# Kernel tuning notes

Measured on AMD Instinct MI355X. Metric: run time of the kernel, lower is better.

Reference implementation:

```python
import jax, jax.numpy as jnp
import numpy as np

N_NODES = 50000
N_EDGES = 600000
FEAT = 128
HID = 128
OUT = 64
N_LAYERS = 4
N_GRAPHS = 128
BN_EPS = 1e-5


def setup_inputs() -> dict:
    key = jax.random.key(0)
    ks = jax.random.split(key, 16)
    x = jax.random.normal(ks[0], (N_NODES, FEAT), dtype=jnp.float32)
    edge_index = jax.random.randint(ks[1], (2, N_EDGES), 0, N_NODES, dtype=jnp.int32)
    batch = jnp.sort(jax.random.randint(ks[2], (N_NODES,), 0, N_GRAPHS, dtype=jnp.int32))
    s = 1.0 / np.sqrt(HID)
    # feat_dim == hidden_dim so all per-layer MLP weights stack to [L, HID, HID]
    W1 = jax.random.normal(ks[3], (N_LAYERS, HID, HID), dtype=jnp.float32) * s
    b1 = jnp.zeros((N_LAYERS, HID), dtype=jnp.float32)
    W2 = jax.random.normal(ks[4], (N_LAYERS, HID, HID), dtype=jnp.float32) * s
    b2 = jnp.zeros((N_LAYERS, HID), dtype=jnp.float32)
    gamma = jnp.ones((N_LAYERS, HID), dtype=jnp.float32)
    beta = jnp.zeros((N_LAYERS, HID), dtype=jnp.float32)
    Wf1 = jax.random.normal(ks[5], (HID, HID), dtype=jnp.float32) * s
    bf1 = jnp.zeros((HID,), dtype=jnp.float32)
    Wf2 = jax.random.normal(ks[6], (HID, OUT), dtype=jnp.float32) * s
    bf2 = jnp.zeros((OUT,), dtype=jnp.float32)
    return {"x": x, "edge_index": edge_index, "batch": batch,
            "W1": W1, "b1": b1, "W2": W2, "b2": b2,
            "gamma": gamma, "beta": beta,
            "Wf1": Wf1, "bf1": bf1, "Wf2": Wf2, "bf2": bf2}


def reference(x, edge_index, batch, W1, b1, W2, b2, gamma, beta, Wf1, bf1, Wf2, bf2):
    src, dst = edge_index[0], edge_index[1]
    h = x
    for l in range(N_LAYERS):
        # GINConv (eps=0): h_i <- MLP(h_i + sum_{j in N(i)} h_j)
        agg = jax.ops.segment_sum(h[src], dst, num_segments=N_NODES)
        h = h + agg
        h = jnp.matmul(jax.nn.relu(jnp.matmul(h, W1[l]) + b1[l]), W2[l]) + b2[l]
        # BatchNorm1d (training mode: batch stats over node dim)
        mean = jnp.mean(h, axis=0)
        var = jnp.var(h, axis=0)
        h = (h - mean) * jax.lax.rsqrt(var + BN_EPS) * gamma[l] + beta[l]
        h = jax.nn.relu(h)
    # global_add_pool over graph ids
    g = jax.ops.segment_sum(h, batch, num_segments=N_GRAPHS)  # [G, HID]
    out = jnp.matmul(jax.nn.relu(jnp.matmul(g, Wf1) + bf1), Wf2) + bf2  # [G, OUT]
    return out
```

## Files before the change

### kernel.cpp

```cpp
#include <hip/hip_runtime.h>

#define NN 50000
#define NE 600000
#define HD 128
#define OUTF 64
#define NL 4
#define NG 128
#define BN_EPS 1e-5f
#define NSB 196

typedef __attribute__((ext_vector_type(8))) short short8v;
typedef __attribute__((ext_vector_type(4))) float float4v;

#define LDSW 136

__device__ inline unsigned short f2bf(float f) {
    unsigned int u = __float_as_uint(f);
    return (unsigned short)((u + 0x7FFF + ((u >> 16) & 1)) >> 16);
}
__device__ inline float bf2f(short s) {
    return __uint_as_float(((unsigned int)(unsigned short)s) << 16);
}

__global__ __launch_bounds__(256) void pack_w_kernel(
    const float* __restrict__ W1, const float* __restrict__ W2,
    short* __restrict__ wpack, float* __restrict__ stats4)
{
    int gid = blockIdx.x * 256 + threadIdx.x;
    if (gid < 256)
        reinterpret_cast<float4*>(stats4)[gid] = (float4){0.f, 0.f, 0.f, 0.f};
    int l  = gid & 63;
    int kb = (gid >> 6) & 3;
    int nt = (gid >> 8) & 7;
    int w  = gid >> 11;
    const float* W = (w & 1) ? (W2 + (size_t)(w >> 1) * HD * HD)
                             : (W1 + (size_t)(w >> 1) * HD * HD);
    int col  = nt * 16 + (l & 15);
    int krow = kb * 32 + (l >> 4) * 8;
    short* o = wpack + (size_t)w * 16384 + ((size_t)(nt * 4 + kb) * 64 + l) * 8;
    #pragma unroll
    for (int i = 0; i < 8; i++)
        o[i] = (short)f2bf(W[(size_t)(krow + i) * HD + col]);
}

__global__ __launch_bounds__(256) void cvt_bf16_kernel(
    const float* __restrict__ x, short* __restrict__ hb)
{
    int idx = blockIdx.x * 256 + threadIdx.x;
    if (idx >= NN * 32) return;
    float4 v = reinterpret_cast<const float4*>(x)[idx];
    short4 o = make_short4((short)f2bf(v.x), (short)f2bf(v.y),
                           (short)f2bf(v.z), (short)f2bf(v.w));
    reinterpret_cast<short4*>(hb)[idx] = o;
}

__global__ __launch_bounds__(512) void layer_kernel(
    const short* __restrict__ hb, const int* __restrict__ row_ptr,
    const int* __restrict__ csr, const short* __restrict__ wp1,
    const float* __restrict__ b1, const short* __restrict__ wp2,
    const float* __restrict__ b2, short* __restrict__ Cb,
    float* __restrict__ sums, float* __restrict__ sumsq)
{
    __shared__ __align__(16) short As[64 * LDSW];
    const int t = threadIdx.x;
    const int row0 = blockIdx.x * 64;

    {
        const int ng = t >> 4;
        const int c8 = (t & 15) * 8;
        #pragma unroll
        for (int it = 0; it < 2; it++) {
            int lr = it * 32 + ng;
            int n = row0 + lr;
            float acc[8] = {0, 0, 0, 0, 0, 0, 0, 0};
            if (n < NN) {
                short8v s = *reinterpret_cast<const short8v*>(&hb[(size_t)n * HD + c8]);
                #pragma unroll
                for (int i = 0; i < 8; i++) acc[i] = bf2f(s[i]);
                int p = row_ptr[n], pe = row_ptr[n + 1];
                for (; p + 2 <= pe; p += 2) {
                    int s0 = csr[p], s1 = csr[p + 1];
                    short8v a = *reinterpret_cast<const short8v*>(&hb[(size_t)s0 * HD + c8]);
                    short8v b = *reinterpret_cast<const short8v*>(&hb[(size_t)s1 * HD + c8]);
                    #pragma unroll
                    for (int i = 0; i < 8; i++) acc[i] += bf2f(a[i]) + bf2f(b[i]);
                }
                if (p < pe) {
                    short8v a = *reinterpret_cast<const short8v*>(&hb[(size_t)csr[p] * HD + c8]);
                    #pragma unroll
                    for (int i = 0; i < 8; i++) acc[i] += bf2f(a[i]);
                }
            }
            short8v o;
            #pragma unroll
            for (int i = 0; i < 8; i++) o[i] = (short)f2bf(acc[i]);
            *reinterpret_cast<short8v*>(&As[lr * LDSW + c8]) = o;
        }
    }
    __syncthreads();

    const int wv = t >> 6, l = t & 63;
    const int l16 = l & 15, lhi = l >> 4;
    const int wrow = (wv >> 1) * 16;
    const int nc0 = (wv & 1) * 4;

    short8v a[4];
    #pragma unroll
    for (int kb = 0; kb < 4; kb++)
        a[kb] = *reinterpret_cast<const short8v*>(&As[(wrow + l16) * LDSW + kb * 32 + lhi * 8]);
    __syncthreads();

    float4v acc[4];
    #pragma unroll
    for (int q = 0; q < 4; q++) acc[q] = (float4v){0.f, 0.f, 0.f, 0.f};
    {
        const short8v* wp = reinterpret_cast<const short8v*>(wp1);
        #pragma unroll
        for (int q = 0; q < 4; q++) {
            int nt = nc0 + q;
            #pragma unroll
            for (int kb = 0; kb < 4; kb++) {
                short8v b = wp[(nt * 4 + kb) * 64 + l];
                acc[q] = __builtin_amdgcn_mfma_f32_16x16x32_bf16(a[kb], b, acc[q], 0, 0, 0);
            }
        }
    }
    #pragma unroll
    for (int q = 0; q < 4; q++) {
        int nt = nc0 + q;
        float bnt = b1[nt * 16 + l16];
        #pragma unroll
        for (int j = 0; j < 4; j++) {
            float v = fmaxf(acc[q][j] + bnt, 0.f);
            As[(wrow + lhi * 4 + j) * LDSW + nt * 16 + l16] = (short)f2bf(v);
        }
    }
    __syncthreads();

    #pragma unroll
    for (int kb = 0; kb < 4; kb++)
        a[kb] = *reinterpret_cast<const short8v*>(&As[(wrow + l16) * LDSW + kb * 32 + lhi * 8]);

    #pragma unroll
    for (int q = 0; q < 4; q++) acc[q] = (float4v){0.f, 0.f, 0.f, 0.f};
    {
        const short8v* wp = reinterpret_cast<const short8v*>(wp2);
        #pragma unroll
        for (int q = 0; q < 4; q++) {
            int nt = nc0 + q;
            #pragma unroll
            for (int kb = 0; kb < 4; kb++) {
                short8v b = wp[(nt * 4 + kb) * 64 + l];
                acc[q] = __builtin_amdgcn_mfma_f32_16x16x32_bf16(a[kb], b, acc[q], 0, 0, 0);
            }
        }
    }

    __syncthreads();
    float* redS = reinterpret_cast<float*>(As);
    float* redQ = redS + 4 * HD;
    #pragma unroll
    for (int q = 0; q < 4; q++) {
        int nt = nc0 + q;
        float bnt = b2[nt * 16 + l16];
        float snt = 0.f, qnt = 0.f;
        #pragma unroll
        for (int j = 0; j < 4; j++) {
            int r = row0 + wrow + lhi * 4 + j;
            if (r < NN) {
                float v = acc[q][j] + bnt;
                Cb[(size_t)r * HD + nt * 16 + l16] = (short)f2bf(v);
                snt += v; qnt += v * v;
            }
        }
        snt += __shfl_xor(snt, 16); snt += __shfl_xor(snt, 32);
        qnt += __shfl_xor(qnt, 16); qnt += __shfl_xor(qnt, 32);
        if (lhi == 0) {
            redS[(wv >> 1) * HD + nt * 16 + l16] = snt;
            redQ[(wv >> 1) * HD + nt * 16 + l16] = qnt;
        }
    }
    __syncthreads();
    if (t < HD) {
        float ss = redS[0 * HD + t] + redS[1 * HD + t] + redS[2 * HD + t] + redS[3 * HD + t];
        float qq = redQ[0 * HD + t] + redQ[1 * HD + t] + redQ[2 * HD + t] + redQ[3 * HD + t];
        atomicAdd(&sums[t], ss);
        atomicAdd(&sumsq[t], qq);
    }
}

__global__ __launch_bounds__(256) void deg_hist_kernel(
    const int* __restrict__ dst, int* __restrict__ deg)
{
    int e = blockIdx.x * 256 + threadIdx.x;
    if (e < NE) atomicAdd(&deg[dst[e]], 1);
}

__global__ __launch_bounds__(256) void scan_partial_kernel(
    const int* __restrict__ deg, int* __restrict__ bsum)
{
    __shared__ int sd[256];
    int t = threadIdx.x;
    int i = blockIdx.x * 256 + t;
    sd[t] = (i < NN) ? deg[i] : 0;
    __syncthreads();
    for (int o = 128; o > 0; o >>= 1) {
        if (t < o) sd[t] += sd[t + o];
        __syncthreads();
    }
    if (t == 0) bsum[blockIdx.x] = sd[0];
}

__global__ __launch_bounds__(256) void scan_bsums_kernel(
    const int* __restrict__ bsum, int* __restrict__ boff)
{
    __shared__ int sd[256];
    int t = threadIdx.x;
    int v = (t < NSB) ? bsum[t] : 0;
    sd[t] = v;
    __syncthreads();
    for (int o = 1; o < 256; o <<= 1) {
        int x = (t >= o) ? sd[t - o] : 0;
        __syncthreads();
        sd[t] += x;
        __syncthreads();
    }
    if (t < NSB) boff[t] = sd[t] - v;
}

__global__ __launch_bounds__(256) void scan_final_kernel(
    const int* __restrict__ deg, const int* __restrict__ boff,
    int* __restrict__ row_ptr, int* __restrict__ cursor)
{
    __shared__ int sd[256];
    int t = threadIdx.x;
    int i = blockIdx.x * 256 + t;
    int v = (i < NN) ? deg[i] : 0;
    sd[t] = v;
    __syncthreads();
    for (int o = 1; o < 256; o <<= 1) {
        int x = (t >= o) ? sd[t - o] : 0;
        __syncthreads();
        sd[t] += x;
        __syncthreads();
    }
    int excl = sd[t] - v + boff[blockIdx.x];
    if (i < NN) { row_ptr[i] = excl; cursor[i] = excl; }
    if (i == NN - 1) row_ptr[NN] = excl + v;
}

__global__ __launch_bounds__(256) void fill_csr_kernel(
    const int* __restrict__ src, const int* __restrict__ dst,
    int* __restrict__ cursor, int* __restrict__ csr)
{
    int e = blockIdx.x * 256 + threadIdx.x;
    if (e >= NE) return;
    int p = atomicAdd(&cursor[dst[e]], 1);
    csr[p] = src[e];
}

__global__ __launch_bounds__(256) void bn_apply_kernel(
    const short* __restrict__ Cb, const float* __restrict__ sums,
    const float* __restrict__ sumsq, const float* __restrict__ gamma,
    const float* __restrict__ beta, short* __restrict__ hb)
{
    __shared__ float sscale[HD];
    __shared__ float sshift[HD];
    int t = threadIdx.x;
    if (t < HD) {
        const float invN = 1.f / (float)NN;
        float mean = sums[t] * invN;
        float var = sumsq[t] * invN - mean * mean;
        float inv = rsqrtf(var + BN_EPS);
        float sc = gamma[t] * inv;
        sscale[t] = sc;
        sshift[t] = beta[t] - mean * sc;
    }
    __syncthreads();
    int idx = blockIdx.x * 256 + t;
    if (idx >= NN * 16) return;
    short8v v = reinterpret_cast<const short8v*>(Cb)[idx];
    int c0 = (idx & 15) * 8;
    short8v o;
    #pragma unroll
    for (int i = 0; i < 8; i++) {
        float f = fmaxf(bf2f(v[i]) * sscale[c0 + i] + sshift[c0 + i], 0.f);
        o[i] = (short)f2bf(f);
    }
    reinterpret_cast<short8v*>(hb)[idx] = o;
}

__global__ __launch_bounds__(256) void pool_kernel_v3(
    const short* __restrict__ hb, const int* __restrict__ batch,
    float* __restrict__ g)
{
    const int gr = blockIdx.x;
    int lo = 0, hi = NN;
    while (lo < hi) { int m = (lo + hi) >> 1; if (batch[m] < gr) lo = m + 1; else hi = m; }
    const int start = lo;
    hi = NN;
    while (lo < hi) { int m = (lo + hi) >> 1; if (batch[m] <= gr) lo = m + 1; else hi = m; }
    const int end = lo;

    const int cg = threadIdx.x & 15;
    const int rg = threadIdx.x >> 4;
    float acc[8] = {0, 0, 0, 0, 0, 0, 0, 0};
    for (int r = start + rg; r < end; r += 16) {
        short8v v = *reinterpret_cast<const short8v*>(&hb[(size_t)r * HD + cg * 8]);
        #pragma unroll
        for (int i = 0; i < 8; i++) acc[i] += bf2f(v[i]);
    }
    __shared__ float red[16][HD];
    #pragma unroll
    for (int i = 0; i < 8; i++) red[rg][cg * 8 + i] = acc[i];
    __syncthreads();
    if (threadIdx.x < HD) {
        float s = 0.f;
        #pragma unroll
        for (int k = 0; k < 16; k++) s += red[k][threadIdx.x];
        g[gr * HD + threadIdx.x] = s;
    }
}

__global__ __launch_bounds__(128) void final_kernel(
    const float* __restrict__ g, const float* __restrict__ Wf1,
    const float* __restrict__ bf1, const float* __restrict__ Wf2,
    const float* __restrict__ bf2, float* __restrict__ out)
{
    __shared__ float gr[HD];
    __shared__ float yr[HD];
    int r = blockIdx.x, c = threadIdx.x;
    gr[c] = g[r * HD + c];
    __syncthreads();
    float acc = bf1[c];
    for (int k = 0; k < HD; k++) acc += gr[k] * Wf1[k * HD + c];
    yr[c] = fmaxf(acc, 0.f);
    __syncthreads();
    if (c < OUTF) {
        float o = bf2[c];
        for (int k = 0; k < HD; k++) o += yr[k] * Wf2[k * OUTF + c];
        out[r * OUTF + c] = o;
    }
}

extern "C" void kernel_launch(void* const* d_in, const int* in_sizes, int n_in,
                              void* d_out, int out_size, void* d_ws, size_t ws_size,
                              hipStream_t stream)
{
    const float* x     = (const float*)d_in[0];
    const int*   ei    = (const int*)  d_in[1];
    const int*   batch = (const int*)  d_in[2];
    const float* W1    = (const float*)d_in[3];
    const float* b1    = (const float*)d_in[4];
    const float* W2    = (const float*)d_in[5];
    const float* b2    = (const float*)d_in[6];
    const float* gamma = (const float*)d_in[7];
    const float* beta  = (const float*)d_in[8];
    const float* Wf1   = (const float*)d_in[9];
    const float* bf1   = (const float*)d_in[10];
    const float* Wf2   = (const float*)d_in[11];
    const float* bf2   = (const float*)d_in[12];
    float* out = (float*)d_out;

    float* ws   = (float*)d_ws;
    const size_t BIG = (size_t)NN * HD;
    short* Cb   = (short*)ws;
    short* hb   = (short*)(ws + BIG);
    float* smal = ws + 3 * BIG;
    float* stats4 = smal;
    float* gpool  = smal + 2048;
    int* ip      = (int*)(smal + 65536);
    int* deg     = ip;
    int* row_ptr = ip + NN;
    int* cursor  = row_ptr + NN + 1;
    int* bsum    = cursor + NN;
    int* boff    = bsum + 256;
    int* csr     = boff + 256;
    short* wpack = (short*)(csr + NE);

    const int* src = ei;
    const int* dst = ei + NE;

    const int layer_grid = (NN + 63) / 64;
    const int cvt_grid  = (NN * 32 + 255) / 256;
    const int bn_grid   = (NN * 16 + 255) / 256;
    const int edge_grid = (NE + 255) / 256;

    pack_w_kernel<<<64, 256, 0, stream>>>(W1, W2, wpack, stats4);
    cvt_bf16_kernel<<<cvt_grid, 256, 0, stream>>>(x, hb);
    hipMemsetAsync(deg, 0, NN * sizeof(int), stream);
    deg_hist_kernel<<<edge_grid, 256, 0, stream>>>(dst, deg);
    scan_partial_kernel<<<NSB, 256, 0, stream>>>(deg, bsum);
    scan_bsums_kernel<<<1, 256, 0, stream>>>(bsum, boff);
    scan_final_kernel<<<NSB, 256, 0, stream>>>(deg, boff, row_ptr, cursor);
    fill_csr_kernel<<<edge_grid, 256, 0, stream>>>(src, dst, cursor, csr);

    for (int l = 0; l < NL; l++) {
        float* sums  = stats4 + l * 256;
        float* sumsq = sums + 128;
        layer_kernel<<<layer_grid, 512, 0, stream>>>(
            hb, row_ptr, csr,
            wpack + (size_t)(l * 2 + 0) * 16384, b1 + l * HD,
            wpack + (size_t)(l * 2 + 1) * 16384, b2 + l * HD,
            Cb, sums, sumsq);
        bn_apply_kernel<<<bn_grid, 256, 0, stream>>>(
            Cb, sums, sumsq, gamma + l * HD, beta + l * HD, hb);
    }

    pool_kernel_v3<<<NG, 256, 0, stream>>>(hb, batch, gpool);
    final_kernel<<<NG, 128, 0, stream>>>(gpool, Wf1, bf1, Wf2, bf2, out);
}
```

Before: 339.4 us.

## Fuse BatchNorm apply and ReLU into next layer's gather and pooling

Removes the separate bn_apply kernel. The BN scale/shift plus ReLU is now applied on the fly when the next layer gathers neighbour features, and in the pooling kernel for the last layer. Layer outputs ping-pong between two buffers. This saves a full read/write pass over the node features per layer and four kernel launches. In exchange, the affine+ReLU is recomputed once per edge in the gather, adding ALU work to a memory-bound loop.

```diff
diff --git a/kernel.cpp b/kernel.cpp
--- a/kernel.cpp
+++ b/kernel.cpp
@@ -54,41 +54,70 @@
     reinterpret_cast<short4*>(hb)[idx] = o;
 }
 
+template<bool BN>
 __global__ __launch_bounds__(512) void layer_kernel(
-    const short* __restrict__ hb, const int* __restrict__ row_ptr,
-    const int* __restrict__ csr, const short* __restrict__ wp1,
-    const float* __restrict__ b1, const short* __restrict__ wp2,
-    const float* __restrict__ b2, short* __restrict__ Cb,
-    float* __restrict__ sums, float* __restrict__ sumsq)
+    const short* __restrict__ inb, const float* __restrict__ stats_prev,
+    const float* __restrict__ gamma_p, const float* __restrict__ beta_p,
+    const int* __restrict__ row_ptr, const int* __restrict__ csr,
+    const short* __restrict__ wp1, const float* __restrict__ b1,
+    const short* __restrict__ wp2, const float* __restrict__ b2,
+    short* __restrict__ Cb, float* __restrict__ sums, float* __restrict__ sumsq)
 {
     __shared__ __align__(16) short As[64 * LDSW];
+    __shared__ float sscale[HD];
+    __shared__ float sshift[HD];
     const int t = threadIdx.x;
     const int row0 = blockIdx.x * 64;
 
+    float sc[8], sh[8];
+    const int c8 = (t & 15) * 8;
+    if (BN) {
+        if (t < HD) {
+            const float invN = 1.f / (float)NN;
+            float mean = stats_prev[t] * invN;
+            float var = stats_prev[HD + t] * invN - mean * mean;
+            float inv = rsqrtf(var + BN_EPS);
+            float s = gamma_p[t] * inv;
+            sscale[t] = s;
+            sshift[t] = beta_p[t] - mean * s;
+        }
+        __syncthreads();
+        #pragma unroll
+        for (int i = 0; i < 8; i++) { sc[i] = sscale[c8 + i]; sh[i] = sshift[c8 + i]; }
+    }
+
     {
         const int ng = t >> 4;
-        const int c8 = (t & 15) * 8;
         #pragma unroll
         for (int it = 0; it < 2; it++) {
             int lr = it * 32 + ng;
             int n = row0 + lr;
             float acc[8] = {0, 0, 0, 0, 0, 0, 0, 0};
             if (n < NN) {
-                short8v s = *reinterpret_cast<const short8v*>(&hb[(size_t)n * HD + c8]);
+                short8v s = *reinterpret_cast<const short8v*>(&inb[(size_t)n * HD + c8]);
                 #pragma unroll
-                for (int i = 0; i < 8; i++) acc[i] = bf2f(s[i]);
+                for (int i = 0; i < 8; i++)
+                    acc[i] = BN ? fmaxf(bf2f(s[i]) * sc[i] + sh[i], 0.f) : bf2f(s[i]);
                 int p = row_ptr[n], pe = row_ptr[n + 1];
                 for (; p + 2 <= pe; p += 2) {
                     int s0 = csr[p], s1 = csr[p + 1];
-                    short8v a = *reinterpret_cast<const short8v*>(&hb[(size_t)s0 * HD + c8]);
-                    short8v b = *reinterpret_cast<const short8v*>(&hb[(size_t)s1 * HD + c8]);
-                    #pragma unroll
-                    for (int i = 0; i < 8; i++) acc[i] += bf2f(a[i]) + bf2f(b[i]);
+                    short8v a = *reinterpret_cast<const short8v*>(&inb[(size_t)s0 * HD + c8]);
+                    short8v b = *reinterpret_cast<const short8v*>(&inb[(size_t)s1 * HD + c8]);
+                    if (BN) {
+                        #pragma unroll
+                        for (int i = 0; i < 8; i++)
+                            acc[i] += fmaxf(bf2f(a[i]) * sc[i] + sh[i], 0.f)
+                                    + fmaxf(bf2f(b[i]) * sc[i] + sh[i], 0.f);
+                    } else {
+                        #pragma unroll
+                        for (int i = 0; i < 8; i++) acc[i] += bf2f(a[i]) + bf2f(b[i]);
+                    }
                 }
                 if (p < pe) {
-                    short8v a = *reinterpret_cast<const short8v*>(&hb[(size_t)csr[p] * HD + c8]);
+                    short8v a = *reinterpret_cast<const short8v*>(&inb[(size_t)csr[p] * HD + c8]);
                     #pragma unroll
-                    for (int i = 0; i < 8; i++) acc[i] += bf2f(a[i]);
+                    for (int i = 0; i < 8; i++)
+                        acc[i] += BN ? fmaxf(bf2f(a[i]) * sc[i] + sh[i], 0.f) : bf2f(a[i]);
                 }
             }
             short8v o;
@@ -259,41 +288,25 @@
     csr[p] = src[e];
 }
 
-__global__ __launch_bounds__(256) void bn_apply_kernel(
-    const short* __restrict__ Cb, const float* __restrict__ sums,
-    const float* __restrict__ sumsq, const float* __restrict__ gamma,
-    const float* __restrict__ beta, short* __restrict__ hb)
+__global__ __launch_bounds__(256) void pool_kernel_v4(
+    const short* __restrict__ Cb, const float* __restrict__ stats,
+    const float* __restrict__ gamma_p, const float* __restrict__ beta_p,
+    const int* __restrict__ batch, float* __restrict__ g)
 {
     __shared__ float sscale[HD];
     __shared__ float sshift[HD];
-    int t = threadIdx.x;
+    const int t = threadIdx.x;
     if (t < HD) {
         const float invN = 1.f / (float)NN;
-        float mean = sums[t] * invN;
-        float var = sumsq[t] * invN - mean * mean;
+        float mean = stats[t] * invN;
+        float var = stats[HD + t] * invN - mean * mean;
         float inv = rsqrtf(var + BN_EPS);
-        float sc = gamma[t] * inv;
-        sscale[t] = sc;
-        sshift[t] = beta[t] - mean * sc;
-    }
-    __syncthreads();
-    int idx = blockIdx.x * 256 + t;
-    if (idx >= NN * 16) return;
-    short8v v = reinterpret_cast<const short8v*>(Cb)[idx];
-    int c0 = (idx & 15) * 8;
-    short8v o;
-    #pragma unroll
-    for (int i = 0; i < 8; i++) {
-        float f = fmaxf(bf2f(v[i]) * sscale[c0 + i] + sshift[c0 + i], 0.f);
-        o[i] = (short)f2bf(f);
-    }
-    reinterpret_cast<short8v*>(hb)[idx] = o;
-}
-
-__global__ __launch_bounds__(256) void pool_kernel_v3(
-    const short* __restrict__ hb, const int* __restrict__ batch,
-    float* __restrict__ g)
-{
+        float s = gamma_p[t] * inv;
+        sscale[t] = s;
+        sshift[t] = beta_p[t] - mean * s;
+    }
+    __syncthreads();
+
     const int gr = blockIdx.x;
     int lo = 0, hi = NN;
     while (lo < hi) { int m = (lo + hi) >> 1; if (batch[m] < gr) lo = m + 1; else hi = m; }
@@ -302,23 +315,28 @@
     while (lo < hi) { int m = (lo + hi) >> 1; if (batch[m] <= gr) lo = m + 1; else hi = m; }
     const int end = lo;
 
-    const int cg = threadIdx.x & 15;
-    const int rg = threadIdx.x >> 4;
+    const int cg = t & 15;
+    const int rg = t >> 4;
+    float sc[8], sh[8];
+    #pragma unroll
+    for (int i = 0; i < 8; i++) { sc[i] = sscale[cg * 8 + i]; sh[i] = sshift[cg * 8 + i]; }
+
     float acc[8] = {0, 0, 0, 0, 0, 0, 0, 0};
     for (int r = start + rg; r < end; r += 16) {
-        short8v v = *reinterpret_cast<const short8v*>(&hb[(size_t)r * HD + cg * 8]);
-        #pragma unroll
-        for (int i = 0; i < 8; i++) acc[i] += bf2f(v[i]);
+        short8v v = *reinterpret_cast<const short8v*>(&Cb[(size_t)r * HD + cg * 8]);
+        #pragma unroll
+        for (int i = 0; i < 8; i++)
+            acc[i] += fmaxf(bf2f(v[i]) * sc[i] + sh[i], 0.f);
     }
     __shared__ float red[16][HD];
     #pragma unroll
     for (int i = 0; i < 8; i++) red[rg][cg * 8 + i] = acc[i];
     __syncthreads();
-    if (threadIdx.x < HD) {
+    if (t < HD) {
         float s = 0.f;
         #pragma unroll
-        for (int k = 0; k < 16; k++) s += red[k][threadIdx.x];
-        g[gr * HD + threadIdx.x] = s;
+        for (int k = 0; k < 16; k++) s += red[k][t];
+        g[gr * HD + t] = s;
     }
 }
 
@@ -364,8 +382,9 @@
 
     float* ws   = (float*)d_ws;
     const size_t BIG = (size_t)NN * HD;
-    short* Cb   = (short*)ws;
-    short* hb   = (short*)(ws + BIG);
+    short* hb  = (short*)ws;
+    short* CbA = (short*)ws + BIG;
+    short* CbB = (short*)ws + 2 * BIG;
     float* smal = ws + 3 * BIG;
     float* stats4 = smal;
     float* gpool  = smal + 2048;
@@ -383,7 +402,6 @@
 
     const int layer_grid = (NN + 63) / 64;
     const int cvt_grid  = (NN * 32 + 255) / 256;
-    const int bn_grid   = (NN * 16 + 255) / 256;
     const int edge_grid = (NE + 255) / 256;
 
     pack_w_kernel<<<64, 256, 0, stream>>>(W1, W2, wpack, stats4);
@@ -395,18 +413,26 @@
     scan_final_kernel<<<NSB, 256, 0, stream>>>(deg, boff, row_ptr, cursor);
     fill_csr_kernel<<<edge_grid, 256, 0, stream>>>(src, dst, cursor, csr);
 
+    const short* lin[NL + 1] = {hb, CbA, CbB, CbA, CbB};
     for (int l = 0; l < NL; l++) {
-        float* sums  = stats4 + l * 256;
-        float* sumsq = sums + 128;
-        layer_kernel<<<layer_grid, 512, 0, stream>>>(
-            hb, row_ptr, csr,
-            wpack + (size_t)(l * 2 + 0) * 16384, b1 + l * HD,
-            wpack + (size_t)(l * 2 + 1) * 16384, b2 + l * HD,
-            Cb, sums, sumsq);
-        bn_apply_kernel<<<bn_grid, 256, 0, stream>>>(
-            Cb, sums, sumsq, gamma + l * HD, beta + l * HD, hb);
-    }
-
-    pool_kernel_v3<<<NG, 256, 0, stream>>>(hb, batch, gpool);
+        float* sums = stats4 + l * 256;
+        if (l == 0) {
+            layer_kernel<false><<<layer_grid, 512, 0, stream>>>(
+                lin[0], nullptr, nullptr, nullptr, row_ptr, csr,
+                wpack + 0 * 16384, b1,
+                wpack + 1 * 16384, b2,
+                (short*)lin[1], sums, sums + 128);
+        } else {
+            layer_kernel<true><<<layer_grid, 512, 0, stream>>>(
+                lin[l], stats4 + (l - 1) * 256, gamma + (l - 1) * HD, beta + (l - 1) * HD,
+                row_ptr, csr,
+                wpack + (size_t)(l * 2 + 0) * 16384, b1 + l * HD,
+                wpack + (size_t)(l * 2 + 1) * 16384, b2 + l * HD,
+                (short*)lin[l + 1], sums, sums + 128);
+        }
+    }
+
+    pool_kernel_v4<<<NG, 256, 0, stream>>>(
+        lin[NL], stats4 + 3 * 256, gamma + 3 * HD, beta + 3 * HD, batch, gpool);
     final_kernel<<<NG, 128, 0, stream>>>(gpool, Wf1, bf1, Wf2, bf2, out);
 }
```

Result: faster. 305.8 us (-9.9%).
